# Kernel tuning notes

Hardware: AMD Instinct MI355X
Metric: run time of the kernel (lower is better)

The kernel has to match this reference:

```python
import jax, jax.numpy as jnp
import numpy as np

B, T, H, S, E, TGT = 8192, 24, 256, 256, 256, 1
IN = 2  # temporal value + mask concatenated


def setup_inputs() -> dict:
    key = jax.random.key(0)
    ks = jax.random.split(key, 20)
    f = jnp.float32
    sc = 0.05
    return {
        "static_feature": jax.random.normal(ks[0], (B, S), f),
        "temporal_feature": jax.random.normal(ks[1], (B, T), f),
        "temporal_mask": (jax.random.uniform(ks[2], (B, T)) < 0.5).astype(f),
        "targets": (jax.random.uniform(ks[3], (B, TGT)) < 0.5).astype(f),
        # fixed random initial hidden/cell state (created in __init__)
        "h0": jax.random.normal(ks[4], (B, H), f),
        "c0": jax.random.normal(ks[5], (B, H), f),
        # LSTMCell params (torch gate order: i, f, g, o)
        "W_ih": jax.random.normal(ks[6], (4 * H, IN), f) * sc,
        "W_hh": jax.random.normal(ks[7], (4 * H, H), f) * sc,
        "b_ih": jax.random.normal(ks[8], (4 * H,), f) * sc,
        "b_hh": jax.random.normal(ks[9], (4 * H,), f) * sc,
        # static-branch MLP
        "W1": jax.random.normal(ks[10], (E, S), f) * sc,
        "b1": jnp.zeros((E,), f),
        "W2": jax.random.normal(ks[11], (E, E), f) * sc,
        "b2": jnp.zeros((E,), f),
        "W3": jax.random.normal(ks[12], (E, E), f) * sc,
        "b3": jnp.zeros((E,), f),
        # final classifier over concat(h, s)
        "W_lr": jax.random.normal(ks[13], (TGT, E + H), f) * sc,
        "b_lr": jnp.zeros((TGT,), f),
    }


def _lstm_step(W_ih, W_hh, b_ih, b_hh):
    def step(carry, xt):
        h, c = carry
        gates = xt @ W_ih.T + b_ih + h @ W_hh.T + b_hh  # [B, 4H]
        i, fg, g, o = jnp.split(gates, 4, axis=-1)
        i = jax.nn.sigmoid(i)
        fg = jax.nn.sigmoid(fg)
        g = jnp.tanh(g)
        o = jax.nn.sigmoid(o)
        c = fg * c + i * g
        h = o * jnp.tanh(c)
        return (h, c), None
    return step


def reference(static_feature, temporal_feature, temporal_mask, targets,
              h0, c0, W_ih, W_hh, b_ih, b_hh,
              W1, b1, W2, b2, W3, b3, W_lr, b_lr):
    # [B, T, 2] -> scan over time: [T, B, 2]
    xs = jnp.swapaxes(jnp.stack([temporal_feature, temporal_mask], axis=-1), 0, 1)
    (h, c), _ = jax.lax.scan(_lstm_step(W_ih, W_hh, b_ih, b_hh), (h0, c0), xs)

    # static MLP (dropout in eval mode = identity)
    s = jax.nn.relu(static_feature @ W1.T + b1)
    s = jax.nn.relu(s @ W2.T + b2)
    s = jax.nn.relu(s @ W3.T + b3)

    predicts = jnp.concatenate([h, s], axis=1) @ W_lr.T + b_lr  # [B, TGT]
    # numerically stable BCEWithLogits, mean reduction
    loss = jnp.mean(jnp.maximum(predicts, 0) - predicts * targets
                    + jnp.log1p(jnp.exp(-jnp.abs(predicts))))
    return predicts, loss
```

## Files before the change

kernel.cpp:

```cpp
#include <hip/hip_runtime.h>

typedef _Float16 f16;
typedef _Float16 f16x8 __attribute__((ext_vector_type(8)));
typedef float f32x16 __attribute__((ext_vector_type(16)));

#define MFMA32(A, B, C) __builtin_amdgcn_mfma_f32_32x32x16_f16((A), (B), (C), 0, 0, 0)

__device__ __forceinline__ float sigm_(float x) {
    return __builtin_amdgcn_rcpf(1.f + __builtin_amdgcn_exp2f(-1.44269504088896f * x));
}
__device__ __forceinline__ float tanh_(float x) {
    float e = __builtin_amdgcn_exp2f(2.88539008177793f * x);
    return 1.f - 2.f * __builtin_amdgcn_rcpf(1.f + e);
}

__device__ __forceinline__ void stage16(const void* g, void* s) {
    __builtin_amdgcn_global_load_lds(
        (const __attribute__((address_space(1))) unsigned int*)(g),
        (__attribute__((address_space(3))) unsigned int*)(s), 16, 0, 0);
}

__global__ void frag_conv_kt(const float* __restrict__ W, f16* __restrict__ dst) {
    int idx = blockIdx.x * blockDim.x + threadIdx.x;
    int e  = idx & 7;
    int lp = (idx >> 3) & 63;
    int nt = (idx >> 9) & 31;
    int kt = idx >> 14;
    int j = (nt << 5) + (lp & 31);
    int k = (kt << 4) + ((lp >> 5) << 3) + e;
    dst[idx] = (f16)W[j * 256 + k];
}

__global__ void frag_conv(const float* __restrict__ W, f16* __restrict__ dst, int total) {
    for (int idx = blockIdx.x * blockDim.x + threadIdx.x; idx < total;
         idx += gridDim.x * blockDim.x) {
        int e  = idx & 7;
        int lp = (idx >> 3) & 63;
        int kt = (idx >> 9) & 15;
        int nt = idx >> 13;
        int j = (nt << 5) + (lp & 31);
        int k = (kt << 4) + ((lp >> 5) << 3) + e;
        dst[idx] = (f16)W[j * 256 + k];
    }
}

#define STAGE4(PN, SRCOFF) do {                                              \
        const char* _g = sb + (SRCOFF);                                      \
        stage16(_g,         (PN) + st_o        );                            \
        stage16(_g +  8192, (PN) + st_o +  4096);                            \
        stage16(_g + 16384, (PN) + st_o +  8192);                            \
        stage16(_g + 24576, (PN) + st_o + 12288);                            \
    } while (0)

#define PHASE(KT, PC, PN) do {                                               \
        asm volatile("s_waitcnt vmcnt(4)" ::: "memory");                     \
        __builtin_amdgcn_s_barrier();                                        \
        __builtin_amdgcn_sched_barrier(0);                                   \
        STAGE4(PN, (((KT) + 2) & 15) * 32768);                               \
        f16x8 Av  = *(const f16x8*)(&Af[KT][l][0]);                          \
        f16x8 Bv0 = *(const f16x8*)((PC) + ((0 * 8 + w) << 9) + (l << 3));   \
        f16x8 Bv1 = *(const f16x8*)((PC) + ((1 * 8 + w) << 9) + (l << 3));   \
        f16x8 Bv2 = *(const f16x8*)((PC) + ((2 * 8 + w) << 9) + (l << 3));   \
        f16x8 Bv3 = *(const f16x8*)((PC) + ((3 * 8 + w) << 9) + (l << 3));   \
        acc0 = MFMA32(Av, Bv0, acc0);                                        \
        acc1 = MFMA32(Av, Bv1, acc1);                                        \
        acc2 = MFMA32(Av, Bv2, acc2);                                        \
        acc3 = MFMA32(Av, Bv3, acc3);                                        \
    } while (0)

__global__ __launch_bounds__(512)
void lstm_fused(const float* __restrict__ statf,
                const float* __restrict__ tfg,
                const float* __restrict__ tmg,
                const float* __restrict__ h0,
                const float* __restrict__ c0,
                const float* __restrict__ Wih,
                const float* __restrict__ bih,
                const float* __restrict__ bhh,
                const float* __restrict__ b1,
                const float* __restrict__ b2,
                const float* __restrict__ b3,
                const float* __restrict__ Wlr,
                const float* __restrict__ blr,
                const f16* __restrict__ WBH,
                const f16* __restrict__ WB1,
                const f16* __restrict__ WB2,
                const f16* __restrict__ WB3,
                float* __restrict__ out)
{
    __shared__ __align__(16) f16 wsl[3][16384];
    __shared__ __align__(16) f16 Af[16][64][8];
    __shared__ float tf_l[32][24];
    __shared__ float tm_l[32][24];
    __shared__ float wlr_l[512];
    __shared__ f16   xa_l[1024];
    __shared__ f16   xb_l[1024];
    __shared__ float xc_l[1024];

    const int tid = threadIdx.x;
    const int w   = tid >> 6;
    const int l   = tid & 63;
    const int b0  = blockIdx.x * 32;

    const char* sb  = (const char*)WBH + (w << 10) + (l << 4);
    const int   st_o = (w << 9) + (l << 3);

    {
        f16* s0 = &wsl[0][0];
        f16* s1 = &wsl[1][0];
        #pragma unroll
        for (int i = 0; i < 4; ++i) stage16(sb + i * 8192,         s0 + st_o + i * 4096);
        #pragma unroll
        for (int i = 0; i < 4; ++i) stage16(sb + 32768 + i * 8192, s1 + st_o + i * 4096);
    }

    for (int i = tid; i < 32 * 24; i += 512) {
        int r = i / 24, t = i - r * 24;
        tf_l[r][t] = tfg[(b0 + r) * 24 + t];
        tm_l[r][t] = tmg[(b0 + r) * 24 + t];
    }
    wlr_l[tid] = Wlr[tid];
    for (int i = tid; i < 1024; i += 512) {
        xa_l[i] = (f16)Wih[2 * i];
        xb_l[i] = (f16)Wih[2 * i + 1];
        xc_l[i] = bih[i] + bhh[i];
    }
    for (int i = tid; i < 1024; i += 512) {
        int fr = i >> 6, lp = i & 63;
        int row  = lp & 31;
        int koff = (fr << 4) + ((lp >> 5) << 3);
        const float4* s4 = (const float4*)&h0[(b0 + row) * 256 + koff];
        float4 a = s4[0], b = s4[1];
        f16x8 v;
        v[0]=(f16)a.x; v[1]=(f16)a.y; v[2]=(f16)a.z; v[3]=(f16)a.w;
        v[4]=(f16)b.x; v[5]=(f16)b.y; v[6]=(f16)b.z; v[7]=(f16)b.w;
        *(f16x8*)(&Af[fr][lp][0]) = v;
    }

    const int jc = (w << 5) + (l & 31);
    float cst[16];
    #pragma unroll
    for (int reg = 0; reg < 16; ++reg) {
        int bl = (reg & 3) + ((reg >> 2) << 3) + ((l >> 5) << 2);
        cst[reg] = c0[(b0 + bl) * 256 + jc];
    }
    const int wkt    = jc >> 4;
    const int wlp_hi = ((l >> 3) & 1) << 5;
    const int we     = l & 7;

    asm volatile("s_waitcnt lgkmcnt(0)" ::: "memory");

    f16* p0 = &wsl[0][0];
    f16* p1 = &wsl[1][0];
    f16* p2 = &wsl[2][0];

    #pragma unroll 1
    for (int t = 0; t < 24; ++t) {
        f32x16 acc0, acc1, acc2, acc3;
        #pragma unroll
        for (int e = 0; e < 16; ++e) { acc0[e] = 0.f; acc1[e] = 0.f; acc2[e] = 0.f; acc3[e] = 0.f; }

        PHASE(0,  p0, p2);  PHASE(1,  p1, p0);  PHASE(2,  p2, p1);
        PHASE(3,  p0, p2);  PHASE(4,  p1, p0);  PHASE(5,  p2, p1);
        PHASE(6,  p0, p2);  PHASE(7,  p1, p0);  PHASE(8,  p2, p1);
        PHASE(9,  p0, p2);  PHASE(10, p1, p0);  PHASE(11, p2, p1);
        PHASE(12, p0, p2);  PHASE(13, p1, p0);  PHASE(14, p2, p1);
        PHASE(15, p0, p2);

        asm volatile("s_waitcnt lgkmcnt(0)" ::: "memory");
        __builtin_amdgcn_s_barrier();
        __builtin_amdgcn_sched_barrier(0);

        float xav0 = (float)xa_l[jc],       xav1 = (float)xa_l[256 + jc];
        float xav2 = (float)xa_l[512 + jc], xav3 = (float)xa_l[768 + jc];
        float xbv0 = (float)xb_l[jc],       xbv1 = (float)xb_l[256 + jc];
        float xbv2 = (float)xb_l[512 + jc], xbv3 = (float)xb_l[768 + jc];
        float xcv0 = xc_l[jc],       xcv1 = xc_l[256 + jc];
        float xcv2 = xc_l[512 + jc], xcv3 = xc_l[768 + jc];
        #pragma unroll
        for (int reg = 0; reg < 16; ++reg) {
            const int   bl  = (reg & 3) + ((reg >> 2) << 3) + ((l >> 5) << 2);
            const float tfv = tf_l[bl][t];
            const float tmv = tm_l[bl][t];
            float gi = acc0[reg] + xav0 * tfv + xbv0 * tmv + xcv0;
            float gf = acc1[reg] + xav1 * tfv + xbv1 * tmv + xcv1;
            float gg = acc2[reg] + xav2 * tfv + xbv2 * tmv + xcv2;
            float go = acc3[reg] + xav3 * tfv + xbv3 * tmv + xcv3;
            float i_ = sigm_(gi);
            float f_ = sigm_(gf);
            float g_ = tanh_(gg);
            float o_ = sigm_(go);
            float c_ = f_ * cst[reg] + i_ * g_;
            cst[reg] = c_;
            float h_ = o_ * tanh_(c_);
            Af[wkt][bl | wlp_hi][we] = (f16)h_;
        }
        asm volatile("s_waitcnt lgkmcnt(0)" ::: "memory");

        f16* tp = p0; p0 = p1; p1 = p2; p2 = tp;
    }

    asm volatile("s_waitcnt vmcnt(0)" ::: "memory");
    __builtin_amdgcn_s_barrier();

    f16* A2 = &wsl[0][0];
    f16* A3 = &wsl[0][8192];

    for (int i = tid; i < 1024; i += 512) {
        int fr = i >> 6, lp = i & 63;
        int row  = lp & 31;
        int koff = (fr << 4) + ((lp >> 5) << 3);
        const float4* s4 = (const float4*)&statf[(b0 + row) * 256 + koff];
        float4 a = s4[0], b = s4[1];
        f16x8 v;
        v[0]=(f16)a.x; v[1]=(f16)a.y; v[2]=(f16)a.z; v[3]=(f16)a.w;
        v[4]=(f16)b.x; v[5]=(f16)b.y; v[6]=(f16)b.z; v[7]=(f16)b.w;
        *(f16x8*)(A2 + ((fr << 6) + lp) * 8) = v;
    }
    __syncthreads();

    {
        const f16*   WBl[3]  = {WB1, WB2, WB3};
        const float* bls[3]  = {b1, b2, b3};
        f16*         ains[3] = {A2, A3, A2};
        f16*         aous[3] = {A3, A2, A3};
        const int lane8 = l << 3;
        #pragma unroll 1
        for (int layer = 0; layer < 3; ++layer) {
            const f16* WL  = WBl[layer];
            f16* ain  = ains[layer];
            f16* aout = aous[layer];
            float bias = bls[layer][jc];
            f32x16 acc2;
            #pragma unroll
            for (int e = 0; e < 16; ++e) acc2[e] = bias;

            f16x8 Bq[2], Aq2[2];
            Bq[0]  = *(const f16x8*)(WL + ((w * 16 + 0) * 512) + lane8);
            Aq2[0] = *(const f16x8*)(ain + (0 * 64 + l) * 8);
            #pragma unroll
            for (int kt = 0; kt < 16; ++kt) {
                const int cb = kt & 1, nb = cb ^ 1;
                if (kt < 15) {
                    Bq[nb]  = *(const f16x8*)(WL + ((w * 16 + (kt + 1)) * 512) + lane8);
                    Aq2[nb] = *(const f16x8*)(ain + ((kt + 1) * 64 + l) * 8);
                }
                acc2 = MFMA32(Aq2[cb], Bq[cb], acc2);
            }
            __syncthreads();
            #pragma unroll
            for (int reg = 0; reg < 16; ++reg) {
                float v = acc2[reg];
                v = v > 0.f ? v : 0.f;
                const int bl2 = (reg & 3) + ((reg >> 2) << 3) + ((l >> 5) << 2);
                aout[(wkt * 64 + (bl2 | wlp_hi)) * 8 + we] = (f16)v;
            }
            __syncthreads();
        }
    }

    {
        const int r  = (w << 2) + (l >> 4);
        const int lg = l & 15;
        const int lp = r | (((lg >> 3) & 1) << 5);
        const int ee = lg & 7;
        float sum = 0.f;
        #pragma unroll
        for (int i = 0; i < 16; ++i) {
            int j = lg + (i << 4);
            float hv = (float)Af[i][lp][ee];
            float sv = (float)A3[(i * 64 + lp) * 8 + ee];
            sum += hv * wlr_l[j] + sv * wlr_l[256 + j];
        }
        sum += __shfl_xor(sum, 8);
        sum += __shfl_xor(sum, 4);
        sum += __shfl_xor(sum, 2);
        sum += __shfl_xor(sum, 1);
        if (lg == 0) out[b0 + r] = sum + blr[0];
    }
}

__global__ __launch_bounds__(1024)
void bce_kernel(const float* __restrict__ pred, const float* __restrict__ tgt,
                float* __restrict__ lossp) {
    const int tid = threadIdx.x;
    float acc = 0.f;
    for (int i = tid; i < 8192; i += 1024) {
        float p  = pred[i];
        float t  = tgt[i];
        float ax = fabsf(p);
        acc += fmaxf(p, 0.f) - p * t
             + log1pf(__builtin_amdgcn_exp2f(-1.44269504088896f * ax));
    }
    #pragma unroll
    for (int m = 32; m >= 1; m >>= 1) acc += __shfl_xor(acc, m);
    __shared__ float red[16];
    if ((tid & 63) == 0) red[tid >> 6] = acc;
    __syncthreads();
    if (tid < 16) {
        float v = red[tid];
        #pragma unroll
        for (int m = 8; m >= 1; m >>= 1) v += __shfl_xor(v, m);
        if (tid == 0) lossp[0] = v * (1.f / 8192.f);
    }
}

extern "C" void kernel_launch(void* const* d_in, const int* in_sizes, int n_in,
                              void* d_out, int out_size, void* d_ws, size_t ws_size,
                              hipStream_t stream) {
    const float* statf = (const float*)d_in[0];
    const float* tfg   = (const float*)d_in[1];
    const float* tmg   = (const float*)d_in[2];
    const float* tgt   = (const float*)d_in[3];
    const float* h0    = (const float*)d_in[4];
    const float* c0    = (const float*)d_in[5];
    const float* Wih   = (const float*)d_in[6];
    const float* Whh   = (const float*)d_in[7];
    const float* bih   = (const float*)d_in[8];
    const float* bhh   = (const float*)d_in[9];
    const float* W1    = (const float*)d_in[10];
    const float* b1    = (const float*)d_in[11];
    const float* W2    = (const float*)d_in[12];
    const float* b2    = (const float*)d_in[13];
    const float* W3    = (const float*)d_in[14];
    const float* b3    = (const float*)d_in[15];
    const float* Wlr   = (const float*)d_in[16];
    const float* blr   = (const float*)d_in[17];
    float* out = (float*)d_out;

    f16* WBH = (f16*)d_ws;
    f16* WB1 = WBH + 262144;
    f16* WB2 = WB1 + 65536;
    f16* WB3 = WB2 + 65536;

    frag_conv_kt<<<512, 512, 0, stream>>>(Whh, WBH);
    frag_conv<<<128, 512, 0, stream>>>(W1, WB1, 65536);
    frag_conv<<<128, 512, 0, stream>>>(W2, WB2, 65536);
    frag_conv<<<128, 512, 0, stream>>>(W3, WB3, 65536);

    lstm_fused<<<256, 512, 0, stream>>>(statf, tfg, tmg, h0, c0, Wih, bih, bhh,
                                        b1, b2, b3, Wlr, blr,
                                        WBH, WB1, WB2, WB3, out);

    bce_kernel<<<1, 1024, 0, stream>>>(out, tgt, out + 8192);
}
```

Before: 316.9 us.

## Drop per-phase barriers, double-buffer hidden state, and swizzle A fragments

Each wave stages and reads only its own weight slices, so the workgroup barrier in every K-phase of the LSTM recurrence is removed and replaced by a per-wave vmcnt wait. The hidden state moves to a ping-pong buffer so a single barrier per timestep covers the h exchange. The A-fragment LDS layout gets an XOR swizzle to cut bank conflicts, and this swizzle is applied consistently in the MLP and classifier stages. The input-projection weights are hoisted out of the time loop and the combined bias seeds the accumulators. The cost is more LDS for the second h buffer and a correctness dependence on per-wave ownership of the staged slices.

```diff
diff --git a/kernel.cpp b/kernel.cpp
--- a/kernel.cpp
+++ b/kernel.cpp
@@ -18,6 +18,10 @@
     __builtin_amdgcn_global_load_lds(
         (const __attribute__((address_space(1))) unsigned int*)(g),
         (__attribute__((address_space(3))) unsigned int*)(s), 16, 0, 0);
+}
+
+__device__ __forceinline__ int afi(int kt, int lp) {
+    return (kt << 6) + (lp ^ (((lp >> 3) ^ kt) & 7));
 }
 
 __global__ void frag_conv_kt(const float* __restrict__ W, f16* __restrict__ dst) {
@@ -53,11 +57,9 @@
     } while (0)
 
 #define PHASE(KT, PC, PN) do {                                               \
-        asm volatile("s_waitcnt vmcnt(4)" ::: "memory");                     \
-        __builtin_amdgcn_s_barrier();                                        \
-        __builtin_amdgcn_sched_barrier(0);                                   \
         STAGE4(PN, (((KT) + 2) & 15) * 32768);                               \
-        f16x8 Av  = *(const f16x8*)(&Af[KT][l][0]);                          \
+        asm volatile("s_waitcnt vmcnt(8)" ::: "memory");                     \
+        f16x8 Av  = *(const f16x8*)(Acur + afi(KT, l) * 8);                  \
         f16x8 Bv0 = *(const f16x8*)((PC) + ((0 * 8 + w) << 9) + (l << 3));   \
         f16x8 Bv1 = *(const f16x8*)((PC) + ((1 * 8 + w) << 9) + (l << 3));   \
         f16x8 Bv2 = *(const f16x8*)((PC) + ((2 * 8 + w) << 9) + (l << 3));   \
@@ -89,7 +91,7 @@
                 float* __restrict__ out)
 {
     __shared__ __align__(16) f16 wsl[3][16384];
-    __shared__ __align__(16) f16 Af[16][64][8];
+    __shared__ __align__(16) f16 Afb[2][1024][8];
     __shared__ float tf_l[32][24];
     __shared__ float tm_l[32][24];
     __shared__ float wlr_l[512];
@@ -134,7 +136,7 @@
         f16x8 v;
         v[0]=(f16)a.x; v[1]=(f16)a.y; v[2]=(f16)a.z; v[3]=(f16)a.w;
         v[4]=(f16)b.x; v[5]=(f16)b.y; v[6]=(f16)b.z; v[7]=(f16)b.w;
-        *(f16x8*)(&Af[fr][lp][0]) = v;
+        *(f16x8*)(&Afb[0][afi(fr, lp)][0]) = v;
     }
 
     const int jc = (w << 5) + (l & 31);
@@ -147,8 +149,15 @@
     const int wkt    = jc >> 4;
     const int wlp_hi = ((l >> 3) & 1) << 5;
     const int we     = l & 7;
+    const float xav0 = (float)xa_l[jc],       xav1 = (float)xa_l[256 + jc];
+    const float xav2 = (float)xa_l[512 + jc], xav3 = (float)xa_l[768 + jc];
+    const float xbv0 = (float)xb_l[jc],       xbv1 = (float)xb_l[256 + jc];
+    const float xbv2 = (float)xb_l[512 + jc], xbv3 = (float)xb_l[768 + jc];
 
     asm volatile("s_waitcnt lgkmcnt(0)" ::: "memory");
+    __builtin_amdgcn_s_barrier();
+    const float xcv0 = xc_l[jc],       xcv1 = xc_l[256 + jc];
+    const float xcv2 = xc_l[512 + jc], xcv3 = xc_l[768 + jc];
 
     f16* p0 = &wsl[0][0];
     f16* p1 = &wsl[1][0];
@@ -156,9 +165,13 @@
 
     #pragma unroll 1
     for (int t = 0; t < 24; ++t) {
+        f16* Acur = &Afb[t & 1][0][0];
+        f16* Anxt = &Afb[(t + 1) & 1][0][0];
         f32x16 acc0, acc1, acc2, acc3;
         #pragma unroll
-        for (int e = 0; e < 16; ++e) { acc0[e] = 0.f; acc1[e] = 0.f; acc2[e] = 0.f; acc3[e] = 0.f; }
+        for (int e = 0; e < 16; ++e) {
+            acc0[e] = xcv0; acc1[e] = xcv1; acc2[e] = xcv2; acc3[e] = xcv3;
+        }
 
         PHASE(0,  p0, p2);  PHASE(1,  p1, p0);  PHASE(2,  p2, p1);
         PHASE(3,  p0, p2);  PHASE(4,  p1, p0);  PHASE(5,  p2, p1);
@@ -167,25 +180,15 @@
         PHASE(12, p0, p2);  PHASE(13, p1, p0);  PHASE(14, p2, p1);
         PHASE(15, p0, p2);
 
-        asm volatile("s_waitcnt lgkmcnt(0)" ::: "memory");
-        __builtin_amdgcn_s_barrier();
-        __builtin_amdgcn_sched_barrier(0);
-
-        float xav0 = (float)xa_l[jc],       xav1 = (float)xa_l[256 + jc];
-        float xav2 = (float)xa_l[512 + jc], xav3 = (float)xa_l[768 + jc];
-        float xbv0 = (float)xb_l[jc],       xbv1 = (float)xb_l[256 + jc];
-        float xbv2 = (float)xb_l[512 + jc], xbv3 = (float)xb_l[768 + jc];
-        float xcv0 = xc_l[jc],       xcv1 = xc_l[256 + jc];
-        float xcv2 = xc_l[512 + jc], xcv3 = xc_l[768 + jc];
         #pragma unroll
         for (int reg = 0; reg < 16; ++reg) {
             const int   bl  = (reg & 3) + ((reg >> 2) << 3) + ((l >> 5) << 2);
             const float tfv = tf_l[bl][t];
             const float tmv = tm_l[bl][t];
-            float gi = acc0[reg] + xav0 * tfv + xbv0 * tmv + xcv0;
-            float gf = acc1[reg] + xav1 * tfv + xbv1 * tmv + xcv1;
-            float gg = acc2[reg] + xav2 * tfv + xbv2 * tmv + xcv2;
-            float go = acc3[reg] + xav3 * tfv + xbv3 * tmv + xcv3;
+            float gi = acc0[reg] + xav0 * tfv + xbv0 * tmv;
+            float gf = acc1[reg] + xav1 * tfv + xbv1 * tmv;
+            float gg = acc2[reg] + xav2 * tfv + xbv2 * tmv;
+            float go = acc3[reg] + xav3 * tfv + xbv3 * tmv;
             float i_ = sigm_(gi);
             float f_ = sigm_(gf);
             float g_ = tanh_(gg);
@@ -193,9 +196,10 @@
             float c_ = f_ * cst[reg] + i_ * g_;
             cst[reg] = c_;
             float h_ = o_ * tanh_(c_);
-            Af[wkt][bl | wlp_hi][we] = (f16)h_;
+            Anxt[afi(wkt, bl | wlp_hi) * 8 + we] = (f16)h_;
         }
         asm volatile("s_waitcnt lgkmcnt(0)" ::: "memory");
+        __builtin_amdgcn_s_barrier();
 
         f16* tp = p0; p0 = p1; p1 = p2; p2 = tp;
     }
@@ -215,7 +219,7 @@
         f16x8 v;
         v[0]=(f16)a.x; v[1]=(f16)a.y; v[2]=(f16)a.z; v[3]=(f16)a.w;
         v[4]=(f16)b.x; v[5]=(f16)b.y; v[6]=(f16)b.z; v[7]=(f16)b.w;
-        *(f16x8*)(A2 + ((fr << 6) + lp) * 8) = v;
+        *(f16x8*)(A2 + afi(fr, lp) * 8) = v;
     }
     __syncthreads();
 
@@ -237,13 +241,13 @@
 
             f16x8 Bq[2], Aq2[2];
             Bq[0]  = *(const f16x8*)(WL + ((w * 16 + 0) * 512) + lane8);
-            Aq2[0] = *(const f16x8*)(ain + (0 * 64 + l) * 8);
+            Aq2[0] = *(const f16x8*)(ain + afi(0, l) * 8);
             #pragma unroll
             for (int kt = 0; kt < 16; ++kt) {
                 const int cb = kt & 1, nb = cb ^ 1;
                 if (kt < 15) {
                     Bq[nb]  = *(const f16x8*)(WL + ((w * 16 + (kt + 1)) * 512) + lane8);
-                    Aq2[nb] = *(const f16x8*)(ain + ((kt + 1) * 64 + l) * 8);
+                    Aq2[nb] = *(const f16x8*)(ain + afi(kt + 1, l) * 8);
                 }
                 acc2 = MFMA32(Aq2[cb], Bq[cb], acc2);
             }
@@ -253,7 +257,7 @@
                 float v = acc2[reg];
                 v = v > 0.f ? v : 0.f;
                 const int bl2 = (reg & 3) + ((reg >> 2) << 3) + ((l >> 5) << 2);
-                aout[(wkt * 64 + (bl2 | wlp_hi)) * 8 + we] = (f16)v;
+                aout[afi(wkt, bl2 | wlp_hi) * 8 + we] = (f16)v;
             }
             __syncthreads();
         }
@@ -268,8 +272,8 @@
         #pragma unroll
         for (int i = 0; i < 16; ++i) {
             int j = lg + (i << 4);
-            float hv = (float)Af[i][lp][ee];
-            float sv = (float)A3[(i * 64 + lp) * 8 + ee];
+            float hv = (float)Afb[0][afi(i, lp)][ee];
+            float sv = (float)A3[afi(i, lp) * 8 + ee];
             sum += hv * wlr_l[j] + sv * wlr_l[256 + j];
         }
         sum += __shfl_xor(sum, 8);
```

Measured after the change: 604.6 us. 90.8% more time.
